# Optimization experiments

Measured on AMD Instinct MI355X. Metric: run time of the kernel, lower is better.

The kernel has to match this reference:

```python
import jax, jax.numpy as jnp
import numpy as np

N = 100000   # nodes
E = 3200000  # edges
IN, HID, OUT = 128, 64, 64
G = 128      # graphs in batch


def setup_inputs() -> dict:
    key = jax.random.key(0)
    ks = jax.random.split(key, 6)
    x = jax.random.normal(ks[0], (N, IN), dtype=jnp.float32)
    edge_index = jax.random.randint(ks[1], (2, E), 0, N, dtype=jnp.int64)
    batch = jnp.sort(jax.random.randint(ks[2], (N,), 0, G, dtype=jnp.int64))
    W1 = jax.random.normal(ks[3], (IN, HID), dtype=jnp.float32) * (1.0 / np.sqrt(IN))
    b1 = jnp.zeros((HID,), dtype=jnp.float32)
    W2 = jax.random.normal(ks[4], (HID + IN, OUT), dtype=jnp.float32) * (1.0 / np.sqrt(HID + IN))
    b2 = jnp.zeros((OUT,), dtype=jnp.float32)
    return {"x": x, "edge_index": edge_index, "batch": batch,
            "W1": W1, "b1": b1, "W2": W2, "b2": b2}


def gcn_conv(x, src, dst, W, b):
    """PyG GCNConv: symmetric normalization with self-loops."""
    h = x @ W  # [N, F_out]
    deg = jax.ops.segment_sum(jnp.ones((E,), h.dtype), dst, num_segments=N) + 1.0
    dinv = jax.lax.rsqrt(deg)  # [N]
    norm = dinv[src] * dinv[dst]  # [E]
    msg = h[src] * norm[:, None]  # [E, F_out]
    agg = jax.ops.segment_sum(msg, dst, num_segments=N)
    agg = agg + h * (dinv * dinv)[:, None]  # self-loop term
    return agg + b


def reference(x, edge_index, batch, W1, b1, W2, b2):
    src, dst = edge_index[0], edge_index[1]
    x1 = x  # original features (float)
    h1 = gcn_conv(x, src, dst, W1, b1)  # [N, HID]
    x2 = h1
    # root of each graph = first node with that batch id (batch is sorted)
    root_idx = jax.ops.segment_min(jnp.arange(N), batch, num_segments=G)
    root_idx = jnp.minimum(root_idx, N - 1)  # guard empty segments
    root1 = x1[root_idx][batch]  # [N, IN]
    h = jax.nn.relu(jnp.concatenate([h1, root1], axis=1))
    # dropout is identity in eval mode
    h = gcn_conv(h, src, dst, W2, b2)  # [N, OUT]
    h = jax.nn.relu(h)
    root2 = x2[root_idx][batch]  # [N, HID]
    h = jnp.concatenate([h, root2], axis=1)  # [N, OUT+HID]
    # scatter_mean over graphs
    sums = jax.ops.segment_sum(h, batch, num_segments=G)
    cnt = jax.ops.segment_sum(jnp.ones((N,), h.dtype), batch, num_segments=G)
    return sums / jnp.maximum(cnt, 1.0)[:, None]  # [G, OUT+HID]
```

## Files before the change

kernel.cpp:

```cpp
#include <hip/hip_runtime.h>
#include <hip/hip_bf16.h>

#define NN 100000
#define NE 3200000
#define FIN 128
#define FH 64
#define FO 64
#define NG 128
#define NP 392
#define PSH 8
#define PMASK 255
#define ECAP 9216
#define OCAP 11264
#define XPAD 136
#define HPAD 72

typedef unsigned short ushort_t;
typedef __attribute__((ext_vector_type(8))) short bf16x8;
typedef __attribute__((ext_vector_type(4))) float f32x4;

__device__ __forceinline__ float bf2f(ushort_t u) {
  unsigned v = ((unsigned)u) << 16;
  float f;
  __builtin_memcpy(&f, &v, 4);
  return f;
}
__device__ __forceinline__ ushort_t f2bf(float f) {
  __hip_bfloat16 b = __float2bfloat16(f);
  ushort_t u;
  __builtin_memcpy(&u, &b, 2);
  return u;
}

__global__ void k_init(int* __restrict__ pcur, float* __restrict__ out,
                       const int* __restrict__ batch, int* __restrict__ root_idx,
                       int* __restrict__ gcnt,
                       ushort_t* __restrict__ psA, ushort_t* __restrict__ psB,
                       const float* __restrict__ W1, const float* __restrict__ W2,
                       ushort_t* __restrict__ wt1, ushort_t* __restrict__ wt2) {
  int i = blockIdx.x * blockDim.x + threadIdx.x;
  if (i < NP) pcur[i] = 0;
  if (i < NG * (FO + FH)) out[i] = 0.0f;
  if (i < FH) {
    psA[(long)NN * FH + i] = 0;
    psB[(long)NN * FH + i] = 0;
  }
  if (i < FH * FIN) {
    int f = i >> 7, k = i & 127;
    wt1[i] = f2bf(W1[k * FH + f]);
  }
  if (i < FH * FO) {
    int f = i >> 6, k = i & 63;
    wt2[i] = f2bf(W2[k * FO + f]);
  }
  if (i < NG) {
    int g = i;
    int lo = 0, hi = NN;
    while (lo < hi) { int m = (lo + hi) >> 1; if (batch[m] < g) lo = m + 1; else hi = m; }
    int a = lo;
    lo = a; hi = NN;
    while (lo < hi) { int m = (lo + hi) >> 1; if (batch[m] < g + 1) lo = m + 1; else hi = m; }
    int b = lo;
    gcnt[g] = b - a;
    root_idx[g] = (b > a) ? a : (NN - 1);
  }
}

__global__ __launch_bounds__(1024) void k_pscatter(const int* __restrict__ ei,
                                                   int* __restrict__ pcur,
                                                   int* __restrict__ part_e) {
  __shared__ int lbase[NP];
  __shared__ int lcur[NP];
  const int EPB = NE / 256;
  int base = blockIdx.x * EPB;
  int tid = threadIdx.x;
  for (int i = tid; i < NP; i += 1024) { lbase[i] = 0; lcur[i] = 0; }
  __syncthreads();
  for (int i = tid; i < EPB; i += 1024) atomicAdd(&lbase[ei[NE + base + i] >> PSH], 1);
  __syncthreads();
  for (int i = tid; i < NP; i += 1024) {
    int c = lbase[i];
    lbase[i] = c ? (i * ECAP + atomicAdd(&pcur[i], c)) : 0;
  }
  __syncthreads();
  for (int i = tid; i < EPB; i += 1024) {
    int s = ei[base + i];
    int d = ei[NE + base + i];
    int p = d >> PSH;
    int pos = atomicAdd(&lcur[p], 1);
    part_e[lbase[p] + pos] = (s << PSH) | (d & PMASK);
  }
}

__global__ __launch_bounds__(256) void k_psort(const int* __restrict__ part_e,
                                               const int* __restrict__ pcur,
                                               int* __restrict__ rowptr,
                                               int* __restrict__ rend,
                                               float* __restrict__ dinv,
                                               int* __restrict__ csr_src) {
  __shared__ int ew[ECAP];
  __shared__ int cnt[256];
  __shared__ int pref[256];
  int p = blockIdx.x, tid = threadIdx.x;
  int pb = p * ECAP;
  int ob = p * OCAP;
  int m = pcur[p];
  for (int i = tid; i < m; i += 256) ew[i] = part_e[pb + i];
  cnt[tid] = 0;
  __syncthreads();
  for (int i = tid; i < m; i += 256) atomicAdd(&cnt[ew[i] & PMASK], 1);
  __syncthreads();
  int deg = cnt[tid];
  int pc = (deg + 15) & ~15;
  pref[tid] = pc;
  __syncthreads();
  for (int d = 1; d < 256; d <<= 1) {
    int t = (tid >= d) ? pref[tid - d] : 0;
    __syncthreads();
    pref[tid] += t;
    __syncthreads();
  }
  int excl = pref[tid] - pc;
  int n = (p << PSH) + tid;
  if (n < NN) {
    rowptr[n] = ob + excl;
    rend[n] = ob + excl + pc;
    dinv[n] = rsqrtf((float)deg + 1.0f);
  }
  for (int j = deg; j < pc; ++j) csr_src[ob + excl + j] = NN;
  __syncthreads();
  pref[tid] = excl;
  __syncthreads();
  for (int i = tid; i < m; i += 256) {
    int w = ew[i];
    int pos = atomicAdd(&pref[w & PMASK], 1);
    csr_src[ob + pos] = w >> PSH;
  }
}

__global__ __launch_bounds__(256) void k_gemm1(const float* __restrict__ x,
                                               const ushort_t* __restrict__ wt1,
                                               const float* __restrict__ dinv,
                                               ushort_t* __restrict__ ps) {
  __shared__ ushort_t Xs[64 * XPAD];
  __shared__ ushort_t Ws[64 * XPAD];
  int tid = threadIdx.x;
  long n0 = (long)blockIdx.x * 64;
  int nvalid = (int)(NN - n0);
  if (nvalid > 64) nvalid = 64;
  for (int idx = tid; idx < 64 * 32; idx += 256) {
    int r = idx >> 5, c4 = (idx & 31) * 4;
    if (r < nvalid) {
      float4 v = *(const float4*)(x + (n0 + r) * FIN + c4);
      ushort4 o;
      o.x = f2bf(v.x); o.y = f2bf(v.y); o.z = f2bf(v.z); o.w = f2bf(v.w);
      *(ushort4*)&Xs[r * XPAD + c4] = o;
    }
  }
  for (int idx = tid; idx < 64 * 16; idx += 256) {
    int r = idx >> 4, c8 = (idx & 15) * 8;
    *(ushort4*)&Ws[r * XPAD + c8]     = *(const ushort4*)(wt1 + r * FIN + c8);
    *(ushort4*)&Ws[r * XPAD + c8 + 4] = *(const ushort4*)(wt1 + r * FIN + c8 + 4);
  }
  __syncthreads();
  int w = tid >> 6, l = tid & 63;
  int nb = w * 16;
  int arow = l & 15, koff = (l >> 4) * 8;
  f32x4 acc0 = {0.f, 0.f, 0.f, 0.f}, acc1 = acc0, acc2 = acc0, acc3 = acc0;
  #pragma unroll
  for (int ks = 0; ks < 4; ++ks) {
    bf16x8 a  = *(const bf16x8*)&Xs[(nb + arow) * XPAD + ks * 32 + koff];
    bf16x8 b0 = *(const bf16x8*)&Ws[(arow +  0) * XPAD + ks * 32 + koff];
    bf16x8 b1 = *(const bf16x8*)&Ws[(arow + 16) * XPAD + ks * 32 + koff];
    bf16x8 b2 = *(const bf16x8*)&Ws[(arow + 32) * XPAD + ks * 32 + koff];
    bf16x8 b3 = *(const bf16x8*)&Ws[(arow + 48) * XPAD + ks * 32 + koff];
    acc0 = __builtin_amdgcn_mfma_f32_16x16x32_bf16(a, b0, acc0, 0, 0, 0);
    acc1 = __builtin_amdgcn_mfma_f32_16x16x32_bf16(a, b1, acc1, 0, 0, 0);
    acc2 = __builtin_amdgcn_mfma_f32_16x16x32_bf16(a, b2, acc2, 0, 0, 0);
    acc3 = __builtin_amdgcn_mfma_f32_16x16x32_bf16(a, b3, acc3, 0, 0, 0);
  }
  int drow = (l >> 4) * 4, dcol = l & 15;
  #pragma unroll
  for (int j = 0; j < 4; ++j) {
    int r = nb + drow + j;
    if (r < nvalid) {
      long n = n0 + r;
      float dn = dinv[n];
      ps[n * FH +  0 + dcol] = f2bf(acc0[j] * dn);
      ps[n * FH + 16 + dcol] = f2bf(acc1[j] * dn);
      ps[n * FH + 32 + dcol] = f2bf(acc2[j] * dn);
      ps[n * FH + 48 + dcol] = f2bf(acc3[j] * dn);
    }
  }
}

__global__ __launch_bounds__(64) void k_rootproj(const float* __restrict__ x,
                                                 const float* __restrict__ W2,
                                                 const int* __restrict__ root_idx,
                                                 float* __restrict__ rp) {
  __shared__ float xr[FIN];
  int g = blockIdx.x;
  int t = threadIdx.x;
  long r = root_idx[g];
  xr[t]      = fmaxf(x[r * FIN + t], 0.0f);
  xr[t + 64] = fmaxf(x[r * FIN + t + 64], 0.0f);
  __syncthreads();
  float acc = 0.0f;
  #pragma unroll 8
  for (int i = 0; i < FIN; ++i) acc += xr[i] * W2[(FH + i) * FO + t];
  rp[g * FO + t] = acc;
}

template <int RELU>
__global__ __launch_bounds__(256) void k_agg(const ushort_t* __restrict__ ps,
                                             const float* __restrict__ dinv,
                                             const int* __restrict__ rowptr,
                                             const int* __restrict__ rend,
                                             const int* __restrict__ csr_src,
                                             const float* __restrict__ bias,
                                             ushort_t* __restrict__ outb) {
  int lane = threadIdx.x & 63;
  int n = __builtin_amdgcn_readfirstlane(blockIdx.x * 4 + (threadIdx.x >> 6));
  int beg = __builtin_amdgcn_readfirstlane(rowptr[n]);
  int end = __builtin_amdgcn_readfirstlane(rend[n]);
  float acc = bf2f(ps[((long)n << 6) + lane]);
  for (int i = beg; i < end; i += 16) {
    int s0 = __builtin_amdgcn_readfirstlane(csr_src[i + 0]);
    int s1 = __builtin_amdgcn_readfirstlane(csr_src[i + 1]);
    int s2 = __builtin_amdgcn_readfirstlane(csr_src[i + 2]);
    int s3 = __builtin_amdgcn_readfirstlane(csr_src[i + 3]);
    int s4 = __builtin_amdgcn_readfirstlane(csr_src[i + 4]);
    int s5 = __builtin_amdgcn_readfirstlane(csr_src[i + 5]);
    int s6 = __builtin_amdgcn_readfirstlane(csr_src[i + 6]);
    int s7 = __builtin_amdgcn_readfirstlane(csr_src[i + 7]);
    int s8 = __builtin_amdgcn_readfirstlane(csr_src[i + 8]);
    int s9 = __builtin_amdgcn_readfirstlane(csr_src[i + 9]);
    int sa = __builtin_amdgcn_readfirstlane(csr_src[i + 10]);
    int sb = __builtin_amdgcn_readfirstlane(csr_src[i + 11]);
    int sc = __builtin_amdgcn_readfirstlane(csr_src[i + 12]);
    int sd = __builtin_amdgcn_readfirstlane(csr_src[i + 13]);
    int se = __builtin_amdgcn_readfirstlane(csr_src[i + 14]);
    int sf = __builtin_amdgcn_readfirstlane(csr_src[i + 15]);
    float v0 = bf2f(ps[((long)s0 << 6) + lane]);
    float v1 = bf2f(ps[((long)s1 << 6) + lane]);
    float v2 = bf2f(ps[((long)s2 << 6) + lane]);
    float v3 = bf2f(ps[((long)s3 << 6) + lane]);
    float v4 = bf2f(ps[((long)s4 << 6) + lane]);
    float v5 = bf2f(ps[((long)s5 << 6) + lane]);
    float v6 = bf2f(ps[((long)s6 << 6) + lane]);
    float v7 = bf2f(ps[((long)s7 << 6) + lane]);
    float v8 = bf2f(ps[((long)s8 << 6) + lane]);
    float v9 = bf2f(ps[((long)s9 << 6) + lane]);
    float va = bf2f(ps[((long)sa << 6) + lane]);
    float vb = bf2f(ps[((long)sb << 6) + lane]);
    float vc = bf2f(ps[((long)sc << 6) + lane]);
    float vd = bf2f(ps[((long)sd << 6) + lane]);
    float ve = bf2f(ps[((long)se << 6) + lane]);
    float vf = bf2f(ps[((long)sf << 6) + lane]);
    acc += v0; acc += v1; acc += v2; acc += v3;
    acc += v4; acc += v5; acc += v6; acc += v7;
    acc += v8; acc += v9; acc += va; acc += vb;
    acc += vc; acc += vd; acc += ve; acc += vf;
  }
  float val = dinv[n] * acc + bias[lane];
  if (RELU) val = fmaxf(val, 0.0f);
  outb[((long)n << 6) + lane] = f2bf(val);
}

__global__ __launch_bounds__(256) void k_gemm2(const ushort_t* __restrict__ h1,
                                               const ushort_t* __restrict__ wt2,
                                               const float* __restrict__ rp,
                                               const int* __restrict__ batch,
                                               const float* __restrict__ dinv,
                                               ushort_t* __restrict__ ps2) {
  __shared__ ushort_t Hs[64 * HPAD];
  __shared__ ushort_t Ws[64 * HPAD];
  int tid = threadIdx.x;
  long n0 = (long)blockIdx.x * 64;
  int nvalid = (int)(NN - n0);
  if (nvalid > 64) nvalid = 64;
  for (int idx = tid; idx < 64 * 16; idx += 256) {
    int r = idx >> 4, c4 = (idx & 15) * 4;
    if (r < nvalid) {
      ushort4 v = *(const ushort4*)(h1 + (n0 + r) * FH + c4);
      ushort4 o;
      o.x = (v.x & 0x8000) ? 0 : v.x;
      o.y = (v.y & 0x8000) ? 0 : v.y;
      o.z = (v.z & 0x8000) ? 0 : v.z;
      o.w = (v.w & 0x8000) ? 0 : v.w;
      *(ushort4*)&Hs[r * HPAD + c4] = o;
    }
  }
  for (int idx = tid; idx < 64 * 16; idx += 256) {
    int r = idx >> 4, c4 = (idx & 15) * 4;
    *(ushort4*)&Ws[r * HPAD + c4] = *(const ushort4*)(wt2 + r * FH + c4);
  }
  __syncthreads();
  int w = tid >> 6, l = tid & 63;
  int nb = w * 16;
  int arow = l & 15, koff = (l >> 4) * 8;
  f32x4 acc0 = {0.f, 0.f, 0.f, 0.f}, acc1 = acc0, acc2 = acc0, acc3 = acc0;
  #pragma unroll
  for (int ks = 0; ks < 2; ++ks) {
    bf16x8 a  = *(const bf16x8*)&Hs[(nb + arow) * HPAD + ks * 32 + koff];
    bf16x8 b0 = *(const bf16x8*)&Ws[(arow +  0) * HPAD + ks * 32 + koff];
    bf16x8 b1 = *(const bf16x8*)&Ws[(arow + 16) * HPAD + ks * 32 + koff];
    bf16x8 b2 = *(const bf16x8*)&Ws[(arow + 32) * HPAD + ks * 32 + koff];
    bf16x8 b3 = *(const bf16x8*)&Ws[(arow + 48) * HPAD + ks * 32 + koff];
    acc0 = __builtin_amdgcn_mfma_f32_16x16x32_bf16(a, b0, acc0, 0, 0, 0);
    acc1 = __builtin_amdgcn_mfma_f32_16x16x32_bf16(a, b1, acc1, 0, 0, 0);
    acc2 = __builtin_amdgcn_mfma_f32_16x16x32_bf16(a, b2, acc2, 0, 0, 0);
    acc3 = __builtin_amdgcn_mfma_f32_16x16x32_bf16(a, b3, acc3, 0, 0, 0);
  }
  int drow = (l >> 4) * 4, dcol = l & 15;
  #pragma unroll
  for (int j = 0; j < 4; ++j) {
    int r = nb + drow + j;
    if (r < nvalid) {
      long n = n0 + r;
      float dn = dinv[n];
      long rb = (long)batch[n] * FO;
      ps2[n * FH +  0 + dcol] = f2bf((acc0[j] + rp[rb +  0 + dcol]) * dn);
      ps2[n * FH + 16 + dcol] = f2bf((acc1[j] + rp[rb + 16 + dcol]) * dn);
      ps2[n * FH + 32 + dcol] = f2bf((acc2[j] + rp[rb + 32 + dcol]) * dn);
      ps2[n * FH + 48 + dcol] = f2bf((acc3[j] + rp[rb + 48 + dcol]) * dn);
    }
  }
}

__global__ __launch_bounds__(64) void k_pool(const ushort_t* __restrict__ r,
                                             const int* __restrict__ batch,
                                             float* __restrict__ out) {
  const int PC = 25;
  int lane = threadIdx.x;
  long n0 = (long)blockIdx.x * PC;
  long n1 = n0 + PC;
  if (n1 > NN) n1 = NN;
  if (n0 >= NN) return;
  float acc = 0.0f;
  int cur = batch[n0];
  for (long n = n0; n < n1; ++n) {
    int g = batch[n];
    if (g != cur) {
      atomicAdd(&out[(long)cur * (FO + FH) + lane], acc);
      acc = 0.0f;
      cur = g;
    }
    acc += bf2f(r[n * FH + lane]);
  }
  atomicAdd(&out[(long)cur * (FO + FH) + lane], acc);
}

__global__ void k_final(float* __restrict__ out, const int* __restrict__ gcnt,
                        const int* __restrict__ root_idx, const ushort_t* __restrict__ h1full) {
  int i = blockIdx.x * blockDim.x + threadIdx.x;
  if (i >= NG * FO) return;
  int g = i >> 6, f = i & 63;
  int c = gcnt[g];
  float inv = 1.0f / fmaxf((float)c, 1.0f);
  out[g * (FO + FH) + f] *= inv;
  out[g * (FO + FH) + FO + f] = (c > 0) ? bf2f(h1full[(long)root_idx[g] * FH + f]) : 0.0f;
}

extern "C" void kernel_launch(void* const* d_in, const int* in_sizes, int n_in,
                              void* d_out, int out_size, void* d_ws, size_t ws_size,
                              hipStream_t stream) {
  const float* x   = (const float*)d_in[0];
  const int*   ei  = (const int*)d_in[1];
  const int*   bat = (const int*)d_in[2];
  const float* W1  = (const float*)d_in[3];
  const float* b1  = (const float*)d_in[4];
  const float* W2  = (const float*)d_in[5];
  const float* b2  = (const float*)d_in[6];
  float* out = (float*)d_out;

  char* p = (char*)d_ws;
  auto carve = [&](size_t bytes) -> void* {
    char* q = p;
    p += (bytes + 511) & ~size_t(511);
    return (void*)q;
  };
  float* dinv    = (float*)carve((size_t)NN * 4);
  int*   pcur    = (int*)carve((size_t)NP * 4);
  int*   part_e  = (int*)carve((size_t)NP * ECAP * 4);
  int*   rowptr  = (int*)carve((size_t)NN * 4);
  int*   rend    = (int*)carve((size_t)NN * 4);
  int*   csr_src = (int*)carve((size_t)NP * OCAP * 4);
  ushort_t* psA  = (ushort_t*)carve((size_t)(NN + 1) * FH * 2);
  ushort_t* psB  = (ushort_t*)carve((size_t)(NN + 1) * FH * 2);
  ushort_t* bufB = (ushort_t*)carve((size_t)NN * FH * 2);
  ushort_t* bufD = (ushort_t*)carve((size_t)NN * FH * 2);
  int*   root_i  = (int*)carve((size_t)NG * 4);
  int*   gcnt    = (int*)carve((size_t)NG * 4);
  float* rp      = (float*)carve((size_t)NG * FO * 4);
  ushort_t* wt1  = (ushort_t*)carve((size_t)FH * FIN * 2);
  ushort_t* wt2  = (ushort_t*)carve((size_t)FH * FO * 2);

  const int GB = (NN + 63) / 64;
  k_init<<<96, 256, 0, stream>>>(pcur, out, bat, root_i, gcnt, psA, psB, W1, W2, wt1, wt2);
  k_pscatter<<<256, 1024, 0, stream>>>(ei, pcur, part_e);
  k_psort<<<NP, 256, 0, stream>>>(part_e, pcur, rowptr, rend, dinv, csr_src);
  k_gemm1<<<GB, 256, 0, stream>>>(x, wt1, dinv, psA);
  k_rootproj<<<NG, 64, 0, stream>>>(x, W2, root_i, rp);
  k_agg<0><<<NN / 4, 256, 0, stream>>>(psA, dinv, rowptr, rend, csr_src, b1, bufB);
  k_gemm2<<<GB, 256, 0, stream>>>(bufB, wt2, rp, bat, dinv, psB);
  k_agg<1><<<NN / 4, 256, 0, stream>>>(psB, dinv, rowptr, rend, csr_src, b2, bufD);
  k_pool<<<(NN + 24) / 25, 64, 0, stream>>>(bufD, bat, out);
  k_final<<<(NG * FO + 255) / 256, 256, 0, stream>>>(out, gcnt, root_i, bufB);
}
```

Measured before the change: 215.9 us.

## Store gathered node features as FP8 and recompute root features in FP32

The per-node feature tables gathered by the two aggregation kernels go from bf16 to FP8 e4m3, halving the bytes pulled per edge in the bandwidth-bound gather. So that the root-node feature output keeps full accuracy, a new kernel recomputes each graph root's first-layer output in FP32 straight from x and W1 over its neighbour list, and the final kernel uses that instead of the bf16 buffer. The cost is much coarser precision in all aggregated messages, which may exceed tolerance, plus one extra small kernel launch.

```diff
diff --git a/kernel.cpp b/kernel.cpp
--- a/kernel.cpp
+++ b/kernel.cpp
@@ -1,5 +1,6 @@
 #include <hip/hip_runtime.h>
 #include <hip/hip_bf16.h>
+#include <hip/hip_fp8.h>
 
 #define NN 100000
 #define NE 3200000
@@ -16,6 +17,7 @@
 #define HPAD 72
 
 typedef unsigned short ushort_t;
+typedef unsigned char u8;
 typedef __attribute__((ext_vector_type(8))) short bf16x8;
 typedef __attribute__((ext_vector_type(4))) float f32x4;
 
@@ -32,18 +34,34 @@
   return u;
 }
 
+__device__ __forceinline__ float fp8dec(u8 b) {
+#if __has_builtin(__builtin_amdgcn_cvt_f32_fp8)
+  return __builtin_amdgcn_cvt_f32_fp8((int)b, 0);
+#else
+  __hip_fp8_e4m3 t; t.__x = b; return (float)t;
+#endif
+}
+__device__ __forceinline__ unsigned fp8pk(float a, float b) {
+#if __has_builtin(__builtin_amdgcn_cvt_pk_fp8_f32)
+  return (unsigned)__builtin_amdgcn_cvt_pk_fp8_f32(a, b, 0, false);
+#else
+  __hip_fp8_e4m3 ta(a), tb(b);
+  return (unsigned)ta.__x | ((unsigned)tb.__x << 8);
+#endif
+}
+
 __global__ void k_init(int* __restrict__ pcur, float* __restrict__ out,
                        const int* __restrict__ batch, int* __restrict__ root_idx,
                        int* __restrict__ gcnt,
-                       ushort_t* __restrict__ psA, ushort_t* __restrict__ psB,
+                       u8* __restrict__ ps8A, u8* __restrict__ ps8B,
                        const float* __restrict__ W1, const float* __restrict__ W2,
                        ushort_t* __restrict__ wt1, ushort_t* __restrict__ wt2) {
   int i = blockIdx.x * blockDim.x + threadIdx.x;
   if (i < NP) pcur[i] = 0;
   if (i < NG * (FO + FH)) out[i] = 0.0f;
   if (i < FH) {
-    psA[(long)NN * FH + i] = 0;
-    psB[(long)NN * FH + i] = 0;
+    ps8A[(long)NN * FH + i] = 0;
+    ps8B[(long)NN * FH + i] = 0;
   }
   if (i < FH * FIN) {
     int f = i >> 7, k = i & 127;
@@ -141,7 +159,7 @@
 __global__ __launch_bounds__(256) void k_gemm1(const float* __restrict__ x,
                                                const ushort_t* __restrict__ wt1,
                                                const float* __restrict__ dinv,
-                                               ushort_t* __restrict__ ps) {
+                                               u8* __restrict__ ps8) {
   __shared__ ushort_t Xs[64 * XPAD];
   __shared__ ushort_t Ws[64 * XPAD];
   int tid = threadIdx.x;
@@ -186,10 +204,12 @@
     if (r < nvalid) {
       long n = n0 + r;
       float dn = dinv[n];
-      ps[n * FH +  0 + dcol] = f2bf(acc0[j] * dn);
-      ps[n * FH + 16 + dcol] = f2bf(acc1[j] * dn);
-      ps[n * FH + 32 + dcol] = f2bf(acc2[j] * dn);
-      ps[n * FH + 48 + dcol] = f2bf(acc3[j] * dn);
+      unsigned u01 = fp8pk(acc0[j] * dn, acc1[j] * dn);
+      unsigned u23 = fp8pk(acc2[j] * dn, acc3[j] * dn);
+      ps8[n * FH +  0 + dcol] = (u8)(u01 & 0xff);
+      ps8[n * FH + 16 + dcol] = (u8)((u01 >> 8) & 0xff);
+      ps8[n * FH + 32 + dcol] = (u8)(u23 & 0xff);
+      ps8[n * FH + 48 + dcol] = (u8)((u23 >> 8) & 0xff);
     }
   }
 }
@@ -211,8 +231,56 @@
   rp[g * FO + t] = acc;
 }
 
+__global__ __launch_bounds__(256) void k_rootfix(const float* __restrict__ x,
+                                                 const float* __restrict__ W1,
+                                                 const float* __restrict__ b1,
+                                                 const float* __restrict__ dinv,
+                                                 const int* __restrict__ root_idx,
+                                                 const int* __restrict__ rowptr,
+                                                 const int* __restrict__ rend,
+                                                 const int* __restrict__ csr_src,
+                                                 float* __restrict__ rootH) {
+  __shared__ float Ws[FIN * FH];
+  __shared__ float part[4 * FH];
+  int g = blockIdx.x, tid = threadIdx.x;
+  for (int i = tid; i < FIN * FH; i += 256) Ws[i] = W1[i];
+  __syncthreads();
+  int rn = root_idx[g];
+  int beg = rowptr[rn], end = rend[rn];
+  int w = tid >> 6, lane = tid & 63;
+  float acc = 0.0f;
+  for (int i = beg + w; i < end; i += 4) {
+    int s = csr_src[i];
+    if (s == NN) continue;
+    float y = 0.0f;
+    #pragma unroll 8
+    for (int k = 0; k < FIN; k += 4) {
+      float4 xv = *(const float4*)(x + (long)s * FIN + k);
+      y += xv.x * Ws[(k + 0) * FH + lane] + xv.y * Ws[(k + 1) * FH + lane]
+         + xv.z * Ws[(k + 2) * FH + lane] + xv.w * Ws[(k + 3) * FH + lane];
+    }
+    acc += y * dinv[s];
+  }
+  if (w == 0) {
+    float y = 0.0f;
+    #pragma unroll 8
+    for (int k = 0; k < FIN; k += 4) {
+      float4 xv = *(const float4*)(x + (long)rn * FIN + k);
+      y += xv.x * Ws[(k + 0) * FH + lane] + xv.y * Ws[(k + 1) * FH + lane]
+         + xv.z * Ws[(k + 2) * FH + lane] + xv.w * Ws[(k + 3) * FH + lane];
+    }
+    acc += y * dinv[rn];
+  }
+  part[w * FH + lane] = acc;
+  __syncthreads();
+  if (tid < FH) {
+    float t = part[tid] + part[FH + tid] + part[2 * FH + tid] + part[3 * FH + tid];
+    rootH[g * FH + tid] = dinv[rn] * t + b1[tid];
+  }
+}
+
 template <int RELU>
-__global__ __launch_bounds__(256) void k_agg(const ushort_t* __restrict__ ps,
+__global__ __launch_bounds__(256) void k_agg(const u8* __restrict__ ps8,
                                              const float* __restrict__ dinv,
                                              const int* __restrict__ rowptr,
                                              const int* __restrict__ rend,
@@ -223,7 +291,7 @@
   int n = __builtin_amdgcn_readfirstlane(blockIdx.x * 4 + (threadIdx.x >> 6));
   int beg = __builtin_amdgcn_readfirstlane(rowptr[n]);
   int end = __builtin_amdgcn_readfirstlane(rend[n]);
-  float acc = bf2f(ps[((long)n << 6) + lane]);
+  float acc = fp8dec(ps8[((long)n << 6) + lane]);
   for (int i = beg; i < end; i += 16) {
     int s0 = __builtin_amdgcn_readfirstlane(csr_src[i + 0]);
     int s1 = __builtin_amdgcn_readfirstlane(csr_src[i + 1]);
@@ -241,26 +309,26 @@
     int sd = __builtin_amdgcn_readfirstlane(csr_src[i + 13]);
     int se = __builtin_amdgcn_readfirstlane(csr_src[i + 14]);
     int sf = __builtin_amdgcn_readfirstlane(csr_src[i + 15]);
-    float v0 = bf2f(ps[((long)s0 << 6) + lane]);
-    float v1 = bf2f(ps[((long)s1 << 6) + lane]);
-    float v2 = bf2f(ps[((long)s2 << 6) + lane]);
-    float v3 = bf2f(ps[((long)s3 << 6) + lane]);
-    float v4 = bf2f(ps[((long)s4 << 6) + lane]);
-    float v5 = bf2f(ps[((long)s5 << 6) + lane]);
-    float v6 = bf2f(ps[((long)s6 << 6) + lane]);
-    float v7 = bf2f(ps[((long)s7 << 6) + lane]);
-    float v8 = bf2f(ps[((long)s8 << 6) + lane]);
-    float v9 = bf2f(ps[((long)s9 << 6) + lane]);
-    float va = bf2f(ps[((long)sa << 6) + lane]);
-    float vb = bf2f(ps[((long)sb << 6) + lane]);
-    float vc = bf2f(ps[((long)sc << 6) + lane]);
-    float vd = bf2f(ps[((long)sd << 6) + lane]);
-    float ve = bf2f(ps[((long)se << 6) + lane]);
-    float vf = bf2f(ps[((long)sf << 6) + lane]);
-    acc += v0; acc += v1; acc += v2; acc += v3;
-    acc += v4; acc += v5; acc += v6; acc += v7;
-    acc += v8; acc += v9; acc += va; acc += vb;
-    acc += vc; acc += vd; acc += ve; acc += vf;
+    u8 c0 = ps8[((long)s0 << 6) + lane];
+    u8 c1 = ps8[((long)s1 << 6) + lane];
+    u8 c2 = ps8[((long)s2 << 6) + lane];
+    u8 c3 = ps8[((long)s3 << 6) + lane];
+    u8 c4 = ps8[((long)s4 << 6) + lane];
+    u8 c5 = ps8[((long)s5 << 6) + lane];
+    u8 c6 = ps8[((long)s6 << 6) + lane];
+    u8 c7 = ps8[((long)s7 << 6) + lane];
+    u8 c8 = ps8[((long)s8 << 6) + lane];
+    u8 c9 = ps8[((long)s9 << 6) + lane];
+    u8 ca = ps8[((long)sa << 6) + lane];
+    u8 cb = ps8[((long)sb << 6) + lane];
+    u8 cc = ps8[((long)sc << 6) + lane];
+    u8 cd = ps8[((long)sd << 6) + lane];
+    u8 ce = ps8[((long)se << 6) + lane];
+    u8 cf = ps8[((long)sf << 6) + lane];
+    acc += fp8dec(c0); acc += fp8dec(c1); acc += fp8dec(c2); acc += fp8dec(c3);
+    acc += fp8dec(c4); acc += fp8dec(c5); acc += fp8dec(c6); acc += fp8dec(c7);
+    acc += fp8dec(c8); acc += fp8dec(c9); acc += fp8dec(ca); acc += fp8dec(cb);
+    acc += fp8dec(cc); acc += fp8dec(cd); acc += fp8dec(ce); acc += fp8dec(cf);
   }
   float val = dinv[n] * acc + bias[lane];
   if (RELU) val = fmaxf(val, 0.0f);
@@ -272,7 +340,7 @@
                                                const float* __restrict__ rp,
                                                const int* __restrict__ batch,
                                                const float* __restrict__ dinv,
-                                               ushort_t* __restrict__ ps2) {
+                                               u8* __restrict__ ps8) {
   __shared__ ushort_t Hs[64 * HPAD];
   __shared__ ushort_t Ws[64 * HPAD];
   int tid = threadIdx.x;
@@ -320,10 +388,14 @@
       long n = n0 + r;
       float dn = dinv[n];
       long rb = (long)batch[n] * FO;
-      ps2[n * FH +  0 + dcol] = f2bf((acc0[j] + rp[rb +  0 + dcol]) * dn);
-      ps2[n * FH + 16 + dcol] = f2bf((acc1[j] + rp[rb + 16 + dcol]) * dn);
-      ps2[n * FH + 32 + dcol] = f2bf((acc2[j] + rp[rb + 32 + dcol]) * dn);
-      ps2[n * FH + 48 + dcol] = f2bf((acc3[j] + rp[rb + 48 + dcol]) * dn);
+      unsigned u01 = fp8pk((acc0[j] + rp[rb +  0 + dcol]) * dn,
+                           (acc1[j] + rp[rb + 16 + dcol]) * dn);
+      unsigned u23 = fp8pk((acc2[j] + rp[rb + 32 + dcol]) * dn,
+                           (acc3[j] + rp[rb + 48 + dcol]) * dn);
+      ps8[n * FH +  0 + dcol] = (u8)(u01 & 0xff);
+      ps8[n * FH + 16 + dcol] = (u8)((u01 >> 8) & 0xff);
+      ps8[n * FH + 32 + dcol] = (u8)(u23 & 0xff);
+      ps8[n * FH + 48 + dcol] = (u8)((u23 >> 8) & 0xff);
     }
   }
 }
@@ -352,14 +424,14 @@
 }
 
 __global__ void k_final(float* __restrict__ out, const int* __restrict__ gcnt,
-                        const int* __restrict__ root_idx, const ushort_t* __restrict__ h1full) {
+                        const float* __restrict__ rootH) {
   int i = blockIdx.x * blockDim.x + threadIdx.x;
   if (i >= NG * FO) return;
   int g = i >> 6, f = i & 63;
   int c = gcnt[g];
   float inv = 1.0f / fmaxf((float)c, 1.0f);
   out[g * (FO + FH) + f] *= inv;
-  out[g * (FO + FH) + FO + f] = (c > 0) ? bf2f(h1full[(long)root_idx[g] * FH + f]) : 0.0f;
+  out[g * (FO + FH) + FO + f] = (c > 0) ? rootH[g * FH + f] : 0.0f;
 }
 
 extern "C" void kernel_launch(void* const* d_in, const int* in_sizes, int n_in,
@@ -386,25 +458,27 @@
   int*   rowptr  = (int*)carve((size_t)NN * 4);
   int*   rend    = (int*)carve((size_t)NN * 4);
   int*   csr_src = (int*)carve((size_t)NP * OCAP * 4);
-  ushort_t* psA  = (ushort_t*)carve((size_t)(NN + 1) * FH * 2);
-  ushort_t* psB  = (ushort_t*)carve((size_t)(NN + 1) * FH * 2);
+  u8*    ps8A    = (u8*)carve((size_t)(NN + 1) * FH);
+  u8*    ps8B    = (u8*)carve((size_t)(NN + 1) * FH);
   ushort_t* bufB = (ushort_t*)carve((size_t)NN * FH * 2);
   ushort_t* bufD = (ushort_t*)carve((size_t)NN * FH * 2);
   int*   root_i  = (int*)carve((size_t)NG * 4);
   int*   gcnt    = (int*)carve((size_t)NG * 4);
   float* rp      = (float*)carve((size_t)NG * FO * 4);
+  float* rootH   = (float*)carve((size_t)NG * FH * 4);
   ushort_t* wt1  = (ushort_t*)carve((size_t)FH * FIN * 2);
   ushort_t* wt2  = (ushort_t*)carve((size_t)FH * FO * 2);
 
   const int GB = (NN + 63) / 64;
-  k_init<<<96, 256, 0, stream>>>(pcur, out, bat, root_i, gcnt, psA, psB, W1, W2, wt1, wt2);
+  k_init<<<96, 256, 0, stream>>>(pcur, out, bat, root_i, gcnt, ps8A, ps8B, W1, W2, wt1, wt2);
   k_pscatter<<<256, 1024, 0, stream>>>(ei, pcur, part_e);
   k_psort<<<NP, 256, 0, stream>>>(part_e, pcur, rowptr, rend, dinv, csr_src);
-  k_gemm1<<<GB, 256, 0, stream>>>(x, wt1, dinv, psA);
+  k_gemm1<<<GB, 256, 0, stream>>>(x, wt1, dinv, ps8A);
   k_rootproj<<<NG, 64, 0, stream>>>(x, W2, root_i, rp);
-  k_agg<0><<<NN / 4, 256, 0, stream>>>(psA, dinv, rowptr, rend, csr_src, b1, bufB);
-  k_gemm2<<<GB, 256, 0, stream>>>(bufB, wt2, rp, bat, dinv, psB);
-  k_agg<1><<<NN / 4, 256, 0, stream>>>(psB, dinv, rowptr, rend, csr_src, b2, bufD);
+  k_rootfix<<<NG, 256, 0, stream>>>(x, W1, b1, dinv, root_i, rowptr, rend, csr_src, rootH);
+  k_agg<0><<<NN / 4, 256, 0, stream>>>(ps8A, dinv, rowptr, rend, csr_src, b1, bufB);
+  k_gemm2<<<GB, 256, 0, stream>>>(bufB, wt2, rp, bat, dinv, ps8B);
+  k_agg<1><<<NN / 4, 256, 0, stream>>>(ps8B, dinv, rowptr, rend, csr_src, b2, bufD);
   k_pool<<<(NN + 24) / 25, 64, 0, stream>>>(bufD, bat, out);
-  k_final<<<(NG * FO + 255) / 256, 256, 0, stream>>>(out, gcnt, root_i, bufB);
-}
+  k_final<<<(NG * FO + 255) / 256, 256, 0, stream>>>(out, gcnt, rootH);
+}
```

Result: slower. 239.2 us (+10.8%).
